# Performance work log

Measured on AMD Instinct MI355X. Metric: run time of the kernel, lower is better.

The kernel has to match this reference:

```python
import jax, jax.numpy as jnp
import numpy as np

N = 50000      # nodes
E = 800000     # edges (before self-loops)
IN = 128       # in_channels
HID = 32       # hidden_channels
H = 4          # num_heads
OUT = 2        # out_channels
NEG_SLOPE = 0.2


def setup_inputs() -> dict:
    key = jax.random.key(0)
    ks = jax.random.split(key, 16)
    s = 0.1
    x = jax.random.normal(ks[0], (N, IN), jnp.float32)
    edge_index = jax.random.randint(ks[1], (2, E), 0, N, dtype=jnp.int32)
    W1 = jax.random.normal(ks[2], (IN, H * HID), jnp.float32) * s
    att_src1 = jax.random.normal(ks[3], (H, HID), jnp.float32) * s
    att_dst1 = jax.random.normal(ks[4], (H, HID), jnp.float32) * s
    b1 = jnp.zeros((H * HID,), jnp.float32)
    W2 = jax.random.normal(ks[5], (H * HID, H * HID), jnp.float32) * s
    att_src2 = jax.random.normal(ks[6], (H, HID), jnp.float32) * s
    att_dst2 = jax.random.normal(ks[7], (H, HID), jnp.float32) * s
    b2 = jnp.zeros((H * HID,), jnp.float32)
    W3 = jax.random.normal(ks[8], (H * HID, OUT), jnp.float32) * s
    att_src3 = jax.random.normal(ks[9], (1, OUT), jnp.float32) * s
    att_dst3 = jax.random.normal(ks[10], (1, OUT), jnp.float32) * s
    b3 = jnp.zeros((OUT,), jnp.float32)
    return {"x": x, "edge_index": edge_index,
            "W1": W1, "att_src1": att_src1, "att_dst1": att_dst1, "b1": b1,
            "W2": W2, "att_src2": att_src2, "att_dst2": att_dst2, "b2": b2,
            "W3": W3, "att_src3": att_src3, "att_dst3": att_dst3, "b3": b3}


def gat_layer(x, src, dst, W, a_src, a_dst, b, heads, ch, concat):
    """PyG GATConv (eval mode): per-edge LeakyReLU attention, edge-softmax over
    incoming edges of each destination node, weighted scatter-add aggregation."""
    n = x.shape[0]
    h = (x @ W).reshape(n, heads, ch)                      # [N,H,C]
    alpha_s = jnp.sum(h * a_src, axis=-1)                  # [N,H]
    alpha_d = jnp.sum(h * a_dst, axis=-1)                  # [N,H]
    alpha = jax.nn.leaky_relu(alpha_s[src] + alpha_d[dst], NEG_SLOPE)  # [E',H]
    amax = jax.ops.segment_max(alpha, dst, num_segments=n)             # [N,H]
    e = jnp.exp(alpha - amax[dst])
    denom = jax.ops.segment_sum(e, dst, num_segments=n)
    w = e / denom[dst]                                     # softmax weights [E',H]
    out = jax.ops.segment_sum(h[src] * w[:, :, None], dst, num_segments=n)  # [N,H,C]
    out = out.reshape(n, heads * ch) if concat else out.mean(axis=1)
    return out + b


def reference(x, edge_index, W1, att_src1, att_dst1, b1,
              W2, att_src2, att_dst2, b2, W3, att_src3, att_dst3, b3):
    # PyG GATConv adds self-loops by default
    loop = jnp.arange(N, dtype=edge_index.dtype)
    src = jnp.concatenate([edge_index[0], loop])
    dst = jnp.concatenate([edge_index[1], loop])
    h = jax.nn.elu(gat_layer(x, src, dst, W1, att_src1, att_dst1, b1, H, HID, True))
    h = jax.nn.elu(gat_layer(h, src, dst, W2, att_src2, att_dst2, b2, H, HID, True))
    h = gat_layer(h, src, dst, W3, att_src3, att_dst3, b3, 1, OUT, False)
    return jax.nn.log_softmax(h, axis=1)
```

## Files before the change

kernel.cpp:

```cpp
#include <hip/hip_runtime.h>
#include <hip/hip_fp16.h>

#define NN 50000
#define EE 800000
#define ET 850000
#define NEG 0.2f
#define SCAN_B 1024
#define NBLK ((NN + SCAN_B - 1) / SCAN_B)
#define GHALF 391
#define RHALF 25024
#define HIST_BLKS ((ET + 255) / 256)

__device__ __forceinline__ float leaky(float x) { return fmaxf(x, NEG * x); }
__device__ __forceinline__ float elu_f(float x) { return x > 0.f ? x : expm1f(x); }

struct alignas(8) half4 { __half2 a, b; };

typedef _Float16 half8_t __attribute__((ext_vector_type(8)));
typedef float float4_t __attribute__((ext_vector_type(4)));

__device__ __forceinline__
void gemm_tile(const float* __restrict__ Xf, const __half* __restrict__ Xh,
               const __half* __restrict__ Wt, __half* __restrict__ Yh,
               int nrows, int row0, int lane,
               const float* __restrict__ att_s, const float* __restrict__ att_d,
               float* __restrict__ asb, float* __restrict__ adb) {
    int n = lane & 15, quad = lane >> 4;
    float atts_r[8], attd_r[8];
#pragma unroll
    for (int t = 0; t < 8; ++t) {
        atts_r[t] = att_s[t * 16 + n];
        attd_r[t] = att_d[t * 16 + n];
    }
    float4_t acc[8];
#pragma unroll
    for (int t = 0; t < 8; ++t) acc[t] = (float4_t){0.f, 0.f, 0.f, 0.f};
    int rA = row0 + n; if (rA >= nrows) rA = nrows - 1;
#pragma unroll
    for (int ch = 0; ch < 4; ++ch) {
        half8_t a;
        if (Xh) {
            a = *(const half8_t*)(Xh + (size_t)rA * 128 + ch * 32 + quad * 8);
        } else {
            const float* xp = Xf + (size_t)rA * 128 + ch * 32 + quad * 8;
            float4 f0 = *(const float4*)xp;
            float4 f1 = *(const float4*)(xp + 4);
            a = (half8_t){(_Float16)f0.x, (_Float16)f0.y, (_Float16)f0.z, (_Float16)f0.w,
                          (_Float16)f1.x, (_Float16)f1.y, (_Float16)f1.z, (_Float16)f1.w};
        }
#pragma unroll
        for (int t = 0; t < 8; ++t) {
            half8_t b = *(const half8_t*)(Wt + (t * 16 + n) * 128 + ch * 32 + quad * 8);
            acc[t] = __builtin_amdgcn_mfma_f32_16x16x32_f16(a, b, acc[t], 0, 0, 0);
        }
    }
#pragma unroll
    for (int rg = 0; rg < 4; ++rg) {
        int row = row0 + quad * 4 + rg;
        if (row < nrows) {
            __half* yp = Yh + (size_t)row * 128 + n;
#pragma unroll
            for (int t = 0; t < 8; ++t)
                yp[t * 16] = __float2half(acc[t][rg]);
        }
    }
#pragma unroll
    for (int rg = 0; rg < 4; ++rg) {
        float ps[4], pd[4];
#pragma unroll
        for (int h = 0; h < 4; ++h) {
            ps[h] = acc[2*h][rg] * atts_r[2*h] + acc[2*h+1][rg] * atts_r[2*h+1];
            pd[h] = acc[2*h][rg] * attd_r[2*h] + acc[2*h+1][rg] * attd_r[2*h+1];
#pragma unroll
            for (int mask = 1; mask < 16; mask <<= 1) {
                ps[h] += __shfl_xor(ps[h], mask, 64);
                pd[h] += __shfl_xor(pd[h], mask, 64);
            }
        }
        int row = row0 + quad * 4 + rg;
        if (n == 0 && row < nrows) {
#pragma unroll
            for (int h = 0; h < 4; ++h) {
                asb[row * 4 + h] = ps[h];
                adb[row * 4 + h] = pd[h];
            }
        }
    }
}

__global__ __launch_bounds__(256)
void gemm_mfma_k(const float* __restrict__ Xf, const __half* __restrict__ Xh,
                 const __half* __restrict__ Wt, __half* __restrict__ Yh, int nrows,
                 const float* __restrict__ att_s, const float* __restrict__ att_d,
                 float* __restrict__ asb, float* __restrict__ adb) {
    int lane = threadIdx.x & 63;
    int wid  = threadIdx.x >> 6;
    int row0 = (blockIdx.x * 4 + wid) * 16;
    if (row0 < nrows)
        gemm_tile(Xf, Xh, Wt, Yh, nrows, row0, lane, att_s, att_d, asb, adb);
}

__global__ __launch_bounds__(256)
void mega_k(const float* __restrict__ Xf, const __half* __restrict__ Wt,
            __half* __restrict__ Yh, int rowBase,
            const float* __restrict__ att_s, const float* __restrict__ att_d,
            float* __restrict__ asb, float* __restrict__ adb,
            int mode,
            const int* __restrict__ ei, int* __restrict__ counts,
            int* __restrict__ rank, const int* __restrict__ rp,
            int* __restrict__ csr) {
    int b = blockIdx.x;
    if (b < GHALF) {
        int lane = threadIdx.x & 63;
        int wid  = threadIdx.x >> 6;
        int row0 = rowBase + (b * 4 + wid) * 16;
        if (row0 < NN)
            gemm_tile(Xf, nullptr, Wt, Yh, NN, row0, lane, att_s, att_d, asb, adb);
    } else {
        int i = (b - GHALF) * 256 + threadIdx.x;
        if (i < ET) {
            if (mode == 0) {
                int dst = (i < EE) ? ei[EE + i] : (i - EE);
                rank[i] = atomicAdd(&counts[dst], 1);
            } else {
                int src, dst;
                if (i < EE) { src = ei[i]; dst = ei[EE + i]; }
                else        { src = dst = i - EE; }
                csr[rp[dst] + rank[i]] = src;
            }
        }
    }
}

__global__ void prep_k(const float* __restrict__ W1, __half* __restrict__ Wt1,
                       const float* __restrict__ W2, __half* __restrict__ Wt2,
                       int* __restrict__ counts) {
    int i = blockIdx.x * 256 + threadIdx.x;
    if (i < 16384) {
        int k = i >> 7, n = i & 127;
        Wt1[n * 128 + k] = __float2half(W1[i]);
    } else if (i < 32768) {
        int j = i - 16384;
        int k = j >> 7, n = j & 127;
        Wt2[n * 128 + k] = __float2half(W2[j]);
    } else {
        int j = i - 32768;
        if (j < NN) counts[j] = 0;
    }
}

__global__ void scan1_k(const int* __restrict__ counts, int* __restrict__ rp,
                        int* __restrict__ bsums) {
    __shared__ int lsum[256];
    int base = blockIdx.x * SCAN_B;
    int v[4];
    int tsum = 0;
#pragma unroll
    for (int j = 0; j < 4; ++j) {
        int i = base + threadIdx.x * 4 + j;
        v[j] = (i < NN) ? counts[i] : 0;
        tsum += v[j];
    }
    lsum[threadIdx.x] = tsum;
    __syncthreads();
    for (int off = 1; off < 256; off <<= 1) {
        int t = (threadIdx.x >= off) ? lsum[threadIdx.x - off] : 0;
        __syncthreads();
        lsum[threadIdx.x] += t;
        __syncthreads();
    }
    int excl = lsum[threadIdx.x] - tsum;
#pragma unroll
    for (int j = 0; j < 4; ++j) {
        int i = base + threadIdx.x * 4 + j;
        if (i < NN) rp[i] = excl;
        excl += v[j];
    }
    if (threadIdx.x == 255) bsums[blockIdx.x] = lsum[255];
}

__global__ void scan23_k(int* __restrict__ rp, const int* __restrict__ bsums) {
    __shared__ int sadd;
    int bx = blockIdx.x;
    if (threadIdx.x < 64) {
        int lane = threadIdx.x;
        int v = (lane < NBLK) ? bsums[lane] : 0;
        for (int off = 1; off < 64; off <<= 1) {
            int t = __shfl_up(v, off, 64);
            if (lane >= off) v += t;
        }
        int srcl = (bx == 0) ? 0 : (bx - 1);
        int ex = __shfl(v, srcl, 64);
        if (lane == 0) sadd = (bx == 0) ? 0 : ex;
        if (bx == 0 && lane == 63) rp[NN] = v;
    }
    __syncthreads();
    int add = sadd;
    int base = bx * SCAN_B + threadIdx.x * 4;
#pragma unroll
    for (int j = 0; j < 4; ++j) {
        int i = base + j;
        if (i < NN) rp[i] += add;
    }
}

__global__ __launch_bounds__(256)
void agg_k(const __half* __restrict__ Hh, const float* __restrict__ asb,
           const float* __restrict__ adb, const int* __restrict__ rp,
           const int* __restrict__ csr, const float* __restrict__ bias,
           __half* __restrict__ Y,
           const float* __restrict__ W3, const float* __restrict__ s3w,
           const float* __restrict__ d3w, float* __restrict__ h3,
           float* __restrict__ as3, float* __restrict__ ad3) {
    int lane = threadIdx.x & 63;
    int hw = lane >> 5;
    int l  = lane & 31;
    int n = blockIdx.x * 8 + (threadIdx.x >> 6) * 2 + hw;
    if (n >= NN) return;
    int hd = l >> 3;
    float ad = adb[n * 4 + hd];
    float acc0 = 0.f, acc1 = 0.f, acc2 = 0.f, acc3 = 0.f, den = 0.f;
    int e = rp[n], end = rp[n + 1], last = end - 1;
    for (int base = e; base < end; base += 8) {
        int s[8]; float a[8]; float2 hraw[8];
#pragma unroll
        for (int j = 0; j < 8; ++j) {
            int i = base + j;
            s[j] = csr[i <= last ? i : last];
        }
#pragma unroll
        for (int j = 0; j < 8; ++j) a[j] = asb[s[j] * 4 + hd] + ad;
#pragma unroll
        for (int j = 0; j < 8; ++j)
            hraw[j] = ((const float2*)(Hh + (size_t)s[j] * 128))[l];
#pragma unroll
        for (int j = 0; j < 8; ++j) {
            float w = __expf(leaky(a[j]));
            w = (base + j <= last) ? w : 0.f;
            den += w;
            const __half2* hp = (const __half2*)&hraw[j];
            float2 f01 = __half22float2(hp[0]);
            float2 f23 = __half22float2(hp[1]);
            acc0 += w * f01.x; acc1 += w * f01.y;
            acc2 += w * f23.x; acc3 += w * f23.y;
        }
    }
    float4 bv = ((const float4*)bias)[l];
    float inv = 1.f / den;
    float o0 = elu_f(acc0 * inv + bv.x);
    float o1 = elu_f(acc1 * inv + bv.y);
    float o2 = elu_f(acc2 * inv + bv.z);
    float o3 = elu_f(acc3 * inv + bv.w);
    if (!W3) {
        half4 hv;
        hv.a = __floats2half2_rn(o0, o1);
        hv.b = __floats2half2_rn(o2, o3);
        ((half4*)(Y + (size_t)n * 128))[l] = hv;
    } else {
        float4 wa = ((const float4*)W3)[l * 2];
        float4 wb = ((const float4*)W3)[l * 2 + 1];
        float p0 = o0 * wa.x + o1 * wa.z + o2 * wb.x + o3 * wb.z;
        float p1 = o0 * wa.y + o1 * wa.w + o2 * wb.y + o3 * wb.w;
        for (int off = 16; off > 0; off >>= 1) {
            p0 += __shfl_down(p0, off, 32);
            p1 += __shfl_down(p1, off, 32);
        }
        if (l == 0) {
            h3[n * 2 + 0] = p0;
            h3[n * 2 + 1] = p1;
            as3[n] = p0 * s3w[0] + p1 * s3w[1];
            ad3[n] = p0 * d3w[0] + p1 * d3w[1];
        }
    }
}

__global__ void l3agg_k(const float* __restrict__ h3, const float* __restrict__ as3,
                        const float* __restrict__ ad3, const int* __restrict__ rp,
                        const int* __restrict__ csr, const float* __restrict__ b3,
                        float* __restrict__ out) {
    int n = blockIdx.x * blockDim.x + threadIdx.x;
    if (n >= NN) return;
    const float2* h2 = (const float2*)h3;
    float adn = ad3[n];
    float den = 0.f, a0 = 0.f, a1 = 0.f;
    int e = rp[n], end = rp[n + 1], last = end - 1;
    for (int base = e; base < end; base += 4) {
        int s[4]; float al[4]; float2 g[4];
#pragma unroll
        for (int j = 0; j < 4; ++j) {
            int i = base + j;
            s[j] = csr[i <= last ? i : last];
        }
#pragma unroll
        for (int j = 0; j < 4; ++j) al[j] = as3[s[j]] + adn;
#pragma unroll
        for (int j = 0; j < 4; ++j) g[j] = h2[s[j]];
#pragma unroll
        for (int j = 0; j < 4; ++j) {
            float w = __expf(leaky(al[j]));
            w = (base + j <= last) ? w : 0.f;
            den += w;
            a0 += w * g[j].x;
            a1 += w * g[j].y;
        }
    }
    float o0 = a0 / den + b3[0];
    float o1 = a1 / den + b3[1];
    float m = fmaxf(o0, o1);
    float lse = m + logf(__expf(o0 - m) + __expf(o1 - m));
    out[n * 2 + 0] = o0 - lse;
    out[n * 2 + 1] = o1 - lse;
}

extern "C" void kernel_launch(void* const* d_in, const int* in_sizes, int n_in,
                              void* d_out, int out_size, void* d_ws, size_t ws_size,
                              hipStream_t stream) {
    const float* x   = (const float*)d_in[0];
    const int*   ei  = (const int*)d_in[1];
    const float* W1  = (const float*)d_in[2];
    const float* as1 = (const float*)d_in[3];
    const float* ad1 = (const float*)d_in[4];
    const float* b1  = (const float*)d_in[5];
    const float* W2  = (const float*)d_in[6];
    const float* as2 = (const float*)d_in[7];
    const float* ad2 = (const float*)d_in[8];
    const float* b2  = (const float*)d_in[9];
    const float* W3  = (const float*)d_in[10];
    const float* s3w = (const float*)d_in[11];
    const float* d3w = (const float*)d_in[12];
    const float* b3  = (const float*)d_in[13];
    float* out = (float*)d_out;

    char* ws = (char*)d_ws;
    size_t off = 0;
    auto alloc = [&](size_t bytes) -> char* {
        char* p = ws + off;
        off = (off + bytes + 255) & ~(size_t)255;
        return p;
    };
    __half* hA    = (__half*)alloc((size_t)NN * 128 * 2);
    __half* hBh   = (__half*)alloc((size_t)NN * 128 * 2);
    float* asb    = (float*)alloc((size_t)NN * 4 * 4);
    float* adb    = (float*)alloc((size_t)NN * 4 * 4);
    int*   rp     = (int*)alloc((size_t)(NN + 1) * 4);
    int*   counts = (int*)alloc((size_t)NN * 4);
    int*   csr    = (int*)alloc((size_t)ET * 4);
    int*   rank   = (int*)alloc((size_t)ET * 4);
    int*   bsums  = (int*)alloc((size_t)NBLK * 4);
    __half* Wt1   = (__half*)alloc(128 * 128 * 2);
    __half* Wt2   = (__half*)alloc(128 * 128 * 2);
    float* h3     = (float*)alloc((size_t)NN * 2 * 4);
    float* s3     = (float*)alloc((size_t)NN * 4);
    float* d3     = (float*)alloc((size_t)NN * 4);

    prep_k<<<(32768 + NN + 255) / 256, 256, 0, stream>>>(W1, Wt1, W2, Wt2, counts);

    mega_k<<<GHALF + HIST_BLKS, 256, 0, stream>>>(x, Wt1, hA, 0, as1, ad1, asb, adb,
                                                  0, ei, counts, rank, nullptr, nullptr);

    scan1_k<<<NBLK, 256, 0, stream>>>(counts, rp, bsums);
    scan23_k<<<NBLK, 256, 0, stream>>>(rp, bsums);

    mega_k<<<GHALF + HIST_BLKS, 256, 0, stream>>>(x, Wt1, hA, RHALF, as1, ad1, asb, adb,
                                                  1, ei, counts, rank, rp, csr);

    agg_k<<<(NN + 7) / 8, 256, 0, stream>>>(hA, asb, adb, rp, csr, b1, hBh,
                                            nullptr, nullptr, nullptr,
                                            nullptr, nullptr, nullptr);

    gemm_mfma_k<<<(NN + 63) / 64, 256, 0, stream>>>(nullptr, hBh, Wt2, hA, NN,
                                                    as2, ad2, asb, adb);

    agg_k<<<(NN + 7) / 8, 256, 0, stream>>>(hA, asb, adb, rp, csr, b2, nullptr,
                                            W3, s3w, d3w, h3, s3, d3);

    l3agg_k<<<(NN + 255) / 256, 256, 0, stream>>>(h3, s3, d3, rp, csr, b3, out);
}
```

Baseline: 268.3 us.

## Overlap layer-1 aggregation tail with layer-2 GEMM in a combined kernel

Layer-1 aggregation is split at node 39040: the first part runs alone, and the remaining nodes are aggregated in the same launch as GEMM tiles for rows already finished (rows below 39040). A final small GEMM launch covers the rest. New buffers hold layer-2 features and attention scores, since hA and asb/adb are still being read while the GEMM writes. The aim is to fill the idle tail of the aggregation and remove a dependency bubble, at the cost of extra workspace and hardcoded split constants.

```diff
diff --git a/kernel.cpp b/kernel.cpp
--- a/kernel.cpp
+++ b/kernel.cpp
@@ -10,6 +10,11 @@
 #define GHALF 391
 #define RHALF 25024
 #define HIST_BLKS ((ET + 255) / 256)
+#define NSPL 39040
+#define A1A_VB 4880
+#define A1B_VB 1370
+#define G2A 610
+#define G2B 172
 
 __device__ __forceinline__ float leaky(float x) { return fmaxf(x, NEG * x); }
 __device__ __forceinline__ float elu_f(float x) { return x > 0.f ? x : expm1f(x); }
@@ -88,14 +93,81 @@
     }
 }
 
+__device__ __forceinline__
+void agg_node(int n, int l, const __half* __restrict__ Hh,
+              const float* __restrict__ asb, const float* __restrict__ adb,
+              const int* __restrict__ rp, const int* __restrict__ csr,
+              const float* __restrict__ bias, __half* __restrict__ Y,
+              const float* __restrict__ W3, const float* __restrict__ s3w,
+              const float* __restrict__ d3w, float* __restrict__ h3,
+              float* __restrict__ as3, float* __restrict__ ad3) {
+    if (n >= NN) return;
+    int hd = l >> 3;
+    float ad = adb[n * 4 + hd];
+    float acc0 = 0.f, acc1 = 0.f, acc2 = 0.f, acc3 = 0.f, den = 0.f;
+    int e = rp[n], end = rp[n + 1], last = end - 1;
+    for (int base = e; base < end; base += 8) {
+        int s[8]; float a[8]; float2 hraw[8];
+#pragma unroll
+        for (int j = 0; j < 8; ++j) {
+            int i = base + j;
+            s[j] = csr[i <= last ? i : last];
+        }
+#pragma unroll
+        for (int j = 0; j < 8; ++j) a[j] = asb[s[j] * 4 + hd] + ad;
+#pragma unroll
+        for (int j = 0; j < 8; ++j)
+            hraw[j] = ((const float2*)(Hh + (size_t)s[j] * 128))[l];
+#pragma unroll
+        for (int j = 0; j < 8; ++j) {
+            float w = __expf(leaky(a[j]));
+            w = (base + j <= last) ? w : 0.f;
+            den += w;
+            const __half2* hp = (const __half2*)&hraw[j];
+            float2 f01 = __half22float2(hp[0]);
+            float2 f23 = __half22float2(hp[1]);
+            acc0 += w * f01.x; acc1 += w * f01.y;
+            acc2 += w * f23.x; acc3 += w * f23.y;
+        }
+    }
+    float4 bv = ((const float4*)bias)[l];
+    float inv = 1.f / den;
+    float o0 = elu_f(acc0 * inv + bv.x);
+    float o1 = elu_f(acc1 * inv + bv.y);
+    float o2 = elu_f(acc2 * inv + bv.z);
+    float o3 = elu_f(acc3 * inv + bv.w);
+    if (!W3) {
+        half4 hv;
+        hv.a = __floats2half2_rn(o0, o1);
+        hv.b = __floats2half2_rn(o2, o3);
+        ((half4*)(Y + (size_t)n * 128))[l] = hv;
+    } else {
+        float4 wa = ((const float4*)W3)[l * 2];
+        float4 wb = ((const float4*)W3)[l * 2 + 1];
+        float p0 = o0 * wa.x + o1 * wa.z + o2 * wb.x + o3 * wb.z;
+        float p1 = o0 * wa.y + o1 * wa.w + o2 * wb.y + o3 * wb.w;
+        for (int off = 16; off > 0; off >>= 1) {
+            p0 += __shfl_down(p0, off, 32);
+            p1 += __shfl_down(p1, off, 32);
+        }
+        if (l == 0) {
+            h3[n * 2 + 0] = p0;
+            h3[n * 2 + 1] = p1;
+            as3[n] = p0 * s3w[0] + p1 * s3w[1];
+            ad3[n] = p0 * d3w[0] + p1 * d3w[1];
+        }
+    }
+}
+
 __global__ __launch_bounds__(256)
 void gemm_mfma_k(const float* __restrict__ Xf, const __half* __restrict__ Xh,
                  const __half* __restrict__ Wt, __half* __restrict__ Yh, int nrows,
+                 int blk0,
                  const float* __restrict__ att_s, const float* __restrict__ att_d,
                  float* __restrict__ asb, float* __restrict__ adb) {
     int lane = threadIdx.x & 63;
     int wid  = threadIdx.x >> 6;
-    int row0 = (blockIdx.x * 4 + wid) * 16;
+    int row0 = ((blk0 + blockIdx.x) * 4 + wid) * 16;
     if (row0 < nrows)
         gemm_tile(Xf, Xh, Wt, Yh, nrows, row0, lane, att_s, att_d, asb, adb);
 }
@@ -132,6 +204,30 @@
     }
 }
 
+__global__ __launch_bounds__(256)
+void mega2_k(const __half* __restrict__ hA, const float* __restrict__ asb,
+             const float* __restrict__ adb, const int* __restrict__ rp,
+             const int* __restrict__ csr, const float* __restrict__ b1,
+             __half* __restrict__ hBh,
+             const __half* __restrict__ Wt2, __half* __restrict__ hC,
+             const float* __restrict__ as2, const float* __restrict__ ad2,
+             float* __restrict__ asb2, float* __restrict__ adb2) {
+    int b = blockIdx.x;
+    int lane = threadIdx.x & 63;
+    if (b < A1B_VB) {
+        int hw = lane >> 5;
+        int l  = lane & 31;
+        int n = NSPL + b * 8 + (threadIdx.x >> 6) * 2 + hw;
+        agg_node(n, l, hA, asb, adb, rp, csr, b1, hBh,
+                 nullptr, nullptr, nullptr, nullptr, nullptr, nullptr);
+    } else {
+        int g = b - A1B_VB;
+        int wid = threadIdx.x >> 6;
+        int row0 = (g * 4 + wid) * 16;
+        gemm_tile(nullptr, hBh, Wt2, hC, NN, row0, lane, as2, ad2, asb2, adb2);
+    }
+}
+
 __global__ void prep_k(const float* __restrict__ W1, __half* __restrict__ Wt1,
                        const float* __restrict__ W2, __half* __restrict__ Wt2,
                        int* __restrict__ counts) {
@@ -205,7 +301,7 @@
 }
 
 __global__ __launch_bounds__(256)
-void agg_k(const __half* __restrict__ Hh, const float* __restrict__ asb,
+void agg_k(int nb0, const __half* __restrict__ Hh, const float* __restrict__ asb,
            const float* __restrict__ adb, const int* __restrict__ rp,
            const int* __restrict__ csr, const float* __restrict__ bias,
            __half* __restrict__ Y,
@@ -215,63 +311,9 @@
     int lane = threadIdx.x & 63;
     int hw = lane >> 5;
     int l  = lane & 31;
-    int n = blockIdx.x * 8 + (threadIdx.x >> 6) * 2 + hw;
-    if (n >= NN) return;
-    int hd = l >> 3;
-    float ad = adb[n * 4 + hd];
-    float acc0 = 0.f, acc1 = 0.f, acc2 = 0.f, acc3 = 0.f, den = 0.f;
-    int e = rp[n], end = rp[n + 1], last = end - 1;
-    for (int base = e; base < end; base += 8) {
-        int s[8]; float a[8]; float2 hraw[8];
-#pragma unroll
-        for (int j = 0; j < 8; ++j) {
-            int i = base + j;
-            s[j] = csr[i <= last ? i : last];
-        }
-#pragma unroll
-        for (int j = 0; j < 8; ++j) a[j] = asb[s[j] * 4 + hd] + ad;
-#pragma unroll
-        for (int j = 0; j < 8; ++j)
-            hraw[j] = ((const float2*)(Hh + (size_t)s[j] * 128))[l];
-#pragma unroll
-        for (int j = 0; j < 8; ++j) {
-            float w = __expf(leaky(a[j]));
-            w = (base + j <= last) ? w : 0.f;
-            den += w;
-            const __half2* hp = (const __half2*)&hraw[j];
-            float2 f01 = __half22float2(hp[0]);
-            float2 f23 = __half22float2(hp[1]);
-            acc0 += w * f01.x; acc1 += w * f01.y;
-            acc2 += w * f23.x; acc3 += w * f23.y;
-        }
-    }
-    float4 bv = ((const float4*)bias)[l];
-    float inv = 1.f / den;
-    float o0 = elu_f(acc0 * inv + bv.x);
-    float o1 = elu_f(acc1 * inv + bv.y);
-    float o2 = elu_f(acc2 * inv + bv.z);
-    float o3 = elu_f(acc3 * inv + bv.w);
-    if (!W3) {
-        half4 hv;
-        hv.a = __floats2half2_rn(o0, o1);
-        hv.b = __floats2half2_rn(o2, o3);
-        ((half4*)(Y + (size_t)n * 128))[l] = hv;
-    } else {
-        float4 wa = ((const float4*)W3)[l * 2];
-        float4 wb = ((const float4*)W3)[l * 2 + 1];
-        float p0 = o0 * wa.x + o1 * wa.z + o2 * wb.x + o3 * wb.z;
-        float p1 = o0 * wa.y + o1 * wa.w + o2 * wb.y + o3 * wb.w;
-        for (int off = 16; off > 0; off >>= 1) {
-            p0 += __shfl_down(p0, off, 32);
-            p1 += __shfl_down(p1, off, 32);
-        }
-        if (l == 0) {
-            h3[n * 2 + 0] = p0;
-            h3[n * 2 + 1] = p1;
-            as3[n] = p0 * s3w[0] + p1 * s3w[1];
-            ad3[n] = p0 * d3w[0] + p1 * d3w[1];
-        }
-    }
+    int n = nb0 + blockIdx.x * 8 + (threadIdx.x >> 6) * 2 + hw;
+    agg_node(n, l, Hh, asb, adb, rp, csr, bias, Y,
+             W3, s3w, d3w, h3, as3, ad3);
 }
 
 __global__ void l3agg_k(const float* __restrict__ h3, const float* __restrict__ as3,
@@ -340,8 +382,11 @@
     };
     __half* hA    = (__half*)alloc((size_t)NN * 128 * 2);
     __half* hBh   = (__half*)alloc((size_t)NN * 128 * 2);
+    __half* hC    = (__half*)alloc((size_t)NN * 128 * 2);
     float* asb    = (float*)alloc((size_t)NN * 4 * 4);
     float* adb    = (float*)alloc((size_t)NN * 4 * 4);
+    float* asb2   = (float*)alloc((size_t)NN * 4 * 4);
+    float* adb2   = (float*)alloc((size_t)NN * 4 * 4);
     int*   rp     = (int*)alloc((size_t)(NN + 1) * 4);
     int*   counts = (int*)alloc((size_t)NN * 4);
     int*   csr    = (int*)alloc((size_t)ET * 4);
@@ -350,8 +395,8 @@
     __half* Wt1   = (__half*)alloc(128 * 128 * 2);
     __half* Wt2   = (__half*)alloc(128 * 128 * 2);
     float* h3     = (float*)alloc((size_t)NN * 2 * 4);
-    float* s3     = (float*)alloc((size_t)NN * 4);
-    float* d3     = (float*)alloc((size_t)NN * 4);
+    float* s3    = (float*)alloc((size_t)NN * 4);
+    float* d3    = (float*)alloc((size_t)NN * 4);
 
     prep_k<<<(32768 + NN + 255) / 256, 256, 0, stream>>>(W1, Wt1, W2, Wt2, counts);
 
@@ -364,14 +409,17 @@
     mega_k<<<GHALF + HIST_BLKS, 256, 0, stream>>>(x, Wt1, hA, RHALF, as1, ad1, asb, adb,
                                                   1, ei, counts, rank, rp, csr);
 
-    agg_k<<<(NN + 7) / 8, 256, 0, stream>>>(hA, asb, adb, rp, csr, b1, hBh,
-                                            nullptr, nullptr, nullptr,
-                                            nullptr, nullptr, nullptr);
-
-    gemm_mfma_k<<<(NN + 63) / 64, 256, 0, stream>>>(nullptr, hBh, Wt2, hA, NN,
-                                                    as2, ad2, asb, adb);
-
-    agg_k<<<(NN + 7) / 8, 256, 0, stream>>>(hA, asb, adb, rp, csr, b2, nullptr,
+    agg_k<<<A1A_VB, 256, 0, stream>>>(0, hA, asb, adb, rp, csr, b1, hBh,
+                                      nullptr, nullptr, nullptr,
+                                      nullptr, nullptr, nullptr);
+
+    mega2_k<<<A1B_VB + G2A, 256, 0, stream>>>(hA, asb, adb, rp, csr, b1, hBh,
+                                              Wt2, hC, as2, ad2, asb2, adb2);
+
+    gemm_mfma_k<<<G2B, 256, 0, stream>>>(nullptr, hBh, Wt2, hC, NN, G2A,
+                                         as2, ad2, asb2, adb2);
+
+    agg_k<<<(NN + 7) / 8, 256, 0, stream>>>(0, hC, asb2, adb2, rp, csr, b2, nullptr,
                                             W3, s3w, d3w, h3, s3, d3);
 
     l3agg_k<<<(NN + 255) / 256, 256, 0, stream>>>(h3, s3, d3, rp, csr, b3, out);
```

Result: no change. 271.5 us (+1.2%).

## Spread layer-1 GEMM across scan kernels and prefetch CSR indices in aggregation

Applied to the files above, without the earlier changes.

The layer-1 GEMM tiles are now spread over four launches (histogram, both scan phases, CSR fill). This fills the otherwise nearly idle scan kernels with useful GEMM work instead of splitting it evenly across two launches. The aggregation and layer-3 kernels software-pipeline the CSR neighbour index loads one batch of 8 ahead, and layer 3 widens its batch from 4 to 8. Layer 2 writes to separate buffers (hC, asb2, adb2), which removes buffer reuse hazards at the cost of extra workspace.

```diff
diff --git a/kernel.cpp b/kernel.cpp
--- a/kernel.cpp
+++ b/kernel.cpp
@@ -7,9 +7,10 @@
 #define NEG 0.2f
 #define SCAN_B 1024
 #define NBLK ((NN + SCAN_B - 1) / SCAN_B)
-#define GHALF 391
-#define RHALF 25024
 #define HIST_BLKS ((ET + 255) / 256)
+#define TA 300
+#define TS 100
+#define TB 282
 
 __device__ __forceinline__ float leaky(float x) { return fmaxf(x, NEG * x); }
 __device__ __forceinline__ float elu_f(float x) { return x > 0.f ? x : expm1f(x); }
@@ -88,47 +89,132 @@
     }
 }
 
-__global__ __launch_bounds__(256)
-void gemm_mfma_k(const float* __restrict__ Xf, const __half* __restrict__ Xh,
-                 const __half* __restrict__ Wt, __half* __restrict__ Yh, int nrows,
-                 const float* __restrict__ att_s, const float* __restrict__ att_d,
-                 float* __restrict__ asb, float* __restrict__ adb) {
-    int lane = threadIdx.x & 63;
-    int wid  = threadIdx.x >> 6;
-    int row0 = (blockIdx.x * 4 + wid) * 16;
-    if (row0 < nrows)
-        gemm_tile(Xf, Xh, Wt, Yh, nrows, row0, lane, att_s, att_d, asb, adb);
-}
-
-__global__ __launch_bounds__(256)
-void mega_k(const float* __restrict__ Xf, const __half* __restrict__ Wt,
-            __half* __restrict__ Yh, int rowBase,
-            const float* __restrict__ att_s, const float* __restrict__ att_d,
-            float* __restrict__ asb, float* __restrict__ adb,
-            int mode,
-            const int* __restrict__ ei, int* __restrict__ counts,
-            int* __restrict__ rank, const int* __restrict__ rp,
-            int* __restrict__ csr) {
-    int b = blockIdx.x;
-    if (b < GHALF) {
-        int lane = threadIdx.x & 63;
-        int wid  = threadIdx.x >> 6;
-        int row0 = rowBase + (b * 4 + wid) * 16;
-        if (row0 < NN)
-            gemm_tile(Xf, nullptr, Wt, Yh, NN, row0, lane, att_s, att_d, asb, adb);
-    } else {
-        int i = (b - GHALF) * 256 + threadIdx.x;
-        if (i < ET) {
-            if (mode == 0) {
-                int dst = (i < EE) ? ei[EE + i] : (i - EE);
-                rank[i] = atomicAdd(&counts[dst], 1);
-            } else {
-                int src, dst;
-                if (i < EE) { src = ei[i]; dst = ei[EE + i]; }
-                else        { src = dst = i - EE; }
-                csr[rp[dst] + rank[i]] = src;
-            }
-        }
+__device__ __forceinline__
+void agg_node(int n, int l, const __half* __restrict__ Hh,
+              const float* __restrict__ asb, const float* __restrict__ adb,
+              const int* __restrict__ rp, const int* __restrict__ csr,
+              const float* __restrict__ bias, __half* __restrict__ Y,
+              const float* __restrict__ W3, const float* __restrict__ s3w,
+              const float* __restrict__ d3w, float* __restrict__ h3,
+              float* __restrict__ as3, float* __restrict__ ad3) {
+    if (n >= NN) return;
+    int hd = l >> 3;
+    float ad = adb[n * 4 + hd];
+    float acc0 = 0.f, acc1 = 0.f, acc2 = 0.f, acc3 = 0.f, den = 0.f;
+    int e = rp[n], end = rp[n + 1], last = end - 1;
+    int s[8];
+#pragma unroll
+    for (int j = 0; j < 8; ++j) {
+        int i = e + j;
+        s[j] = csr[i <= last ? i : last];
+    }
+    for (int base = e; base < end; base += 8) {
+        float a[8]; float2 hraw[8]; int sN[8];
+#pragma unroll
+        for (int j = 0; j < 8; ++j)
+            hraw[j] = ((const float2*)(Hh + (size_t)s[j] * 128))[l];
+#pragma unroll
+        for (int j = 0; j < 8; ++j) a[j] = asb[s[j] * 4 + hd] + ad;
+        int nb = base + 8;
+#pragma unroll
+        for (int j = 0; j < 8; ++j) {
+            int i = nb + j;
+            sN[j] = csr[i <= last ? i : last];
+        }
+#pragma unroll
+        for (int j = 0; j < 8; ++j) {
+            float w = __expf(leaky(a[j]));
+            w = (base + j <= last) ? w : 0.f;
+            den += w;
+            const __half2* hp = (const __half2*)&hraw[j];
+            float2 f01 = __half22float2(hp[0]);
+            float2 f23 = __half22float2(hp[1]);
+            acc0 += w * f01.x; acc1 += w * f01.y;
+            acc2 += w * f23.x; acc3 += w * f23.y;
+        }
+#pragma unroll
+        for (int j = 0; j < 8; ++j) s[j] = sN[j];
+    }
+    float4 bv = ((const float4*)bias)[l];
+    float inv = 1.f / den;
+    float o0 = elu_f(acc0 * inv + bv.x);
+    float o1 = elu_f(acc1 * inv + bv.y);
+    float o2 = elu_f(acc2 * inv + bv.z);
+    float o3 = elu_f(acc3 * inv + bv.w);
+    if (!W3) {
+        half4 hv;
+        hv.a = __floats2half2_rn(o0, o1);
+        hv.b = __floats2half2_rn(o2, o3);
+        ((half4*)(Y + (size_t)n * 128))[l] = hv;
+    } else {
+        float4 wa = ((const float4*)W3)[l * 2];
+        float4 wb = ((const float4*)W3)[l * 2 + 1];
+        float p0 = o0 * wa.x + o1 * wa.z + o2 * wb.x + o3 * wb.z;
+        float p1 = o0 * wa.y + o1 * wa.w + o2 * wb.y + o3 * wb.w;
+        for (int off = 16; off > 0; off >>= 1) {
+            p0 += __shfl_down(p0, off, 32);
+            p1 += __shfl_down(p1, off, 32);
+        }
+        if (l == 0) {
+            h3[n * 2 + 0] = p0;
+            h3[n * 2 + 1] = p1;
+            as3[n] = p0 * s3w[0] + p1 * s3w[1];
+            ad3[n] = p0 * d3w[0] + p1 * d3w[1];
+        }
+    }
+}
+
+__device__ __forceinline__
+void scan1_f(const int* __restrict__ counts, int* __restrict__ rp,
+             int* __restrict__ bsums, int bx, int tid, int* lsum) {
+    int base = bx * SCAN_B;
+    int v[4]; int tsum = 0;
+#pragma unroll
+    for (int j = 0; j < 4; ++j) {
+        int i = base + tid * 4 + j;
+        v[j] = (i < NN) ? counts[i] : 0;
+        tsum += v[j];
+    }
+    lsum[tid] = tsum;
+    __syncthreads();
+    for (int off = 1; off < 256; off <<= 1) {
+        int t = (tid >= off) ? lsum[tid - off] : 0;
+        __syncthreads();
+        lsum[tid] += t;
+        __syncthreads();
+    }
+    int excl = lsum[tid] - tsum;
+#pragma unroll
+    for (int j = 0; j < 4; ++j) {
+        int i = base + tid * 4 + j;
+        if (i < NN) rp[i] = excl;
+        excl += v[j];
+    }
+    if (tid == 255) bsums[bx] = lsum[255];
+}
+
+__device__ __forceinline__
+void scan23_f(int* __restrict__ rp, const int* __restrict__ bsums,
+              int bx, int tid, int* psadd) {
+    if (tid < 64) {
+        int ln = tid;
+        int v = (ln < NBLK) ? bsums[ln] : 0;
+        for (int off = 1; off < 64; off <<= 1) {
+            int t = __shfl_up(v, off, 64);
+            if (ln >= off) v += t;
+        }
+        int srcl = (bx == 0) ? 0 : (bx - 1);
+        int ex = __shfl(v, srcl, 64);
+        if (ln == 0) *psadd = (bx == 0) ? 0 : ex;
+        if (bx == 0 && ln == 63) rp[NN] = v;
+    }
+    __syncthreads();
+    int add = *psadd;
+    int base = bx * SCAN_B + tid * 4;
+#pragma unroll
+    for (int j = 0; j < 4; ++j) {
+        int i = base + j;
+        if (i < NN) rp[i] += add;
     }
 }
 
@@ -149,59 +235,100 @@
     }
 }
 
-__global__ void scan1_k(const int* __restrict__ counts, int* __restrict__ rp,
-                        int* __restrict__ bsums) {
+__global__ __launch_bounds__(256)
+void megaA_k(const float* __restrict__ x, const __half* __restrict__ Wt1,
+             __half* __restrict__ hA,
+             const float* __restrict__ as1, const float* __restrict__ ad1,
+             float* __restrict__ asb, float* __restrict__ adb,
+             const int* __restrict__ ei, int* __restrict__ counts,
+             int* __restrict__ rank) {
+    int b = blockIdx.x;
+    if (b < TA) {
+        int lane = threadIdx.x & 63;
+        int wid  = threadIdx.x >> 6;
+        int row0 = (b * 4 + wid) * 16;
+        gemm_tile(x, nullptr, Wt1, hA, NN, row0, lane, as1, ad1, asb, adb);
+    } else {
+        int i = (b - TA) * 256 + threadIdx.x;
+        if (i < ET) {
+            int dst = (i < EE) ? ei[EE + i] : (i - EE);
+            rank[i] = atomicAdd(&counts[dst], 1);
+        }
+    }
+}
+
+__global__ __launch_bounds__(256)
+void megaS1_k(const int* __restrict__ counts, int* __restrict__ rp,
+              int* __restrict__ bsums,
+              const float* __restrict__ x, const __half* __restrict__ Wt1,
+              __half* __restrict__ hA,
+              const float* __restrict__ as1, const float* __restrict__ ad1,
+              float* __restrict__ asb, float* __restrict__ adb) {
     __shared__ int lsum[256];
-    int base = blockIdx.x * SCAN_B;
-    int v[4];
-    int tsum = 0;
-#pragma unroll
-    for (int j = 0; j < 4; ++j) {
-        int i = base + threadIdx.x * 4 + j;
-        v[j] = (i < NN) ? counts[i] : 0;
-        tsum += v[j];
-    }
-    lsum[threadIdx.x] = tsum;
-    __syncthreads();
-    for (int off = 1; off < 256; off <<= 1) {
-        int t = (threadIdx.x >= off) ? lsum[threadIdx.x - off] : 0;
-        __syncthreads();
-        lsum[threadIdx.x] += t;
-        __syncthreads();
-    }
-    int excl = lsum[threadIdx.x] - tsum;
-#pragma unroll
-    for (int j = 0; j < 4; ++j) {
-        int i = base + threadIdx.x * 4 + j;
-        if (i < NN) rp[i] = excl;
-        excl += v[j];
-    }
-    if (threadIdx.x == 255) bsums[blockIdx.x] = lsum[255];
-}
-
-__global__ void scan23_k(int* __restrict__ rp, const int* __restrict__ bsums) {
+    int b = blockIdx.x;
+    if (b < NBLK) {
+        scan1_f(counts, rp, bsums, b, threadIdx.x, lsum);
+    } else {
+        int lane = threadIdx.x & 63;
+        int wid  = threadIdx.x >> 6;
+        int row0 = ((TA + b - NBLK) * 4 + wid) * 16;
+        gemm_tile(x, nullptr, Wt1, hA, NN, row0, lane, as1, ad1, asb, adb);
+    }
+}
+
+__global__ __launch_bounds__(256)
+void megaS2_k(int* __restrict__ rp, const int* __restrict__ bsums,
+              const float* __restrict__ x, const __half* __restrict__ Wt1,
+              __half* __restrict__ hA,
+              const float* __restrict__ as1, const float* __restrict__ ad1,
+              float* __restrict__ asb, float* __restrict__ adb) {
     __shared__ int sadd;
-    int bx = blockIdx.x;
-    if (threadIdx.x < 64) {
-        int lane = threadIdx.x;
-        int v = (lane < NBLK) ? bsums[lane] : 0;
-        for (int off = 1; off < 64; off <<= 1) {
-            int t = __shfl_up(v, off, 64);
-            if (lane >= off) v += t;
-        }
-        int srcl = (bx == 0) ? 0 : (bx - 1);
-        int ex = __shfl(v, srcl, 64);
-        if (lane == 0) sadd = (bx == 0) ? 0 : ex;
-        if (bx == 0 && lane == 63) rp[NN] = v;
-    }
-    __syncthreads();
-    int add = sadd;
-    int base = bx * SCAN_B + threadIdx.x * 4;
-#pragma unroll
-    for (int j = 0; j < 4; ++j) {
-        int i = base + j;
-        if (i < NN) rp[i] += add;
-    }
+    int b = blockIdx.x;
+    if (b < NBLK) {
+        scan23_f(rp, bsums, b, threadIdx.x, &sadd);
+    } else {
+        int lane = threadIdx.x & 63;
+        int wid  = threadIdx.x >> 6;
+        int row0 = ((TA + TS + b - NBLK) * 4 + wid) * 16;
+        gemm_tile(x, nullptr, Wt1, hA, NN, row0, lane, as1, ad1, asb, adb);
+    }
+}
+
+__global__ __launch_bounds__(256)
+void megaB_k(const float* __restrict__ x, const __half* __restrict__ Wt1,
+             __half* __restrict__ hA,
+             const float* __restrict__ as1, const float* __restrict__ ad1,
+             float* __restrict__ asb, float* __restrict__ adb,
+             const int* __restrict__ ei, const int* __restrict__ rp,
+             const int* __restrict__ rank, int* __restrict__ csr) {
+    int b = blockIdx.x;
+    if (b < TB) {
+        int lane = threadIdx.x & 63;
+        int wid  = threadIdx.x >> 6;
+        int row0 = ((TA + 2 * TS + b) * 4 + wid) * 16;
+        if (row0 < NN)
+            gemm_tile(x, nullptr, Wt1, hA, NN, row0, lane, as1, ad1, asb, adb);
+    } else {
+        int i = (b - TB) * 256 + threadIdx.x;
+        if (i < ET) {
+            int src, dst;
+            if (i < EE) { src = ei[i]; dst = ei[EE + i]; }
+            else        { src = dst = i - EE; }
+            csr[rp[dst] + rank[i]] = src;
+        }
+    }
+}
+
+__global__ __launch_bounds__(256)
+void gemm_mfma_k(const __half* __restrict__ Xh, const __half* __restrict__ Wt,
+                 __half* __restrict__ Yh,
+                 const float* __restrict__ att_s, const float* __restrict__ att_d,
+                 float* __restrict__ asb, float* __restrict__ adb) {
+    int lane = threadIdx.x & 63;
+    int wid  = threadIdx.x >> 6;
+    int row0 = (blockIdx.x * 4 + wid) * 16;
+    if (row0 < NN)
+        gemm_tile(nullptr, Xh, Wt, Yh, NN, row0, lane, att_s, att_d, asb, adb);
 }
 
 __global__ __launch_bounds__(256)
@@ -216,62 +343,8 @@
     int hw = lane >> 5;
     int l  = lane & 31;
     int n = blockIdx.x * 8 + (threadIdx.x >> 6) * 2 + hw;
-    if (n >= NN) return;
-    int hd = l >> 3;
-    float ad = adb[n * 4 + hd];
-    float acc0 = 0.f, acc1 = 0.f, acc2 = 0.f, acc3 = 0.f, den = 0.f;
-    int e = rp[n], end = rp[n + 1], last = end - 1;
-    for (int base = e; base < end; base += 8) {
-        int s[8]; float a[8]; float2 hraw[8];
-#pragma unroll
-        for (int j = 0; j < 8; ++j) {
-            int i = base + j;
-            s[j] = csr[i <= last ? i : last];
-        }
-#pragma unroll
-        for (int j = 0; j < 8; ++j) a[j] = asb[s[j] * 4 + hd] + ad;
-#pragma unroll
-        for (int j = 0; j < 8; ++j)
-            hraw[j] = ((const float2*)(Hh + (size_t)s[j] * 128))[l];
-#pragma unroll
-        for (int j = 0; j < 8; ++j) {
-            float w = __expf(leaky(a[j]));
-            w = (base + j <= last) ? w : 0.f;
-            den += w;
-            const __half2* hp = (const __half2*)&hraw[j];
-            float2 f01 = __half22float2(hp[0]);
-            float2 f23 = __half22float2(hp[1]);
-            acc0 += w * f01.x; acc1 += w * f01.y;
-            acc2 += w * f23.x; acc3 += w * f23.y;
-        }
-    }
-    float4 bv = ((const float4*)bias)[l];
-    float inv = 1.f / den;
-    float o0 = elu_f(acc0 * inv + bv.x);
-    float o1 = elu_f(acc1 * inv + bv.y);
-    float o2 = elu_f(acc2 * inv + bv.z);
-    float o3 = elu_f(acc3 * inv + bv.w);
-    if (!W3) {
-        half4 hv;
-        hv.a = __floats2half2_rn(o0, o1);
-        hv.b = __floats2half2_rn(o2, o3);
-        ((half4*)(Y + (size_t)n * 128))[l] = hv;
-    } else {
-        float4 wa = ((const float4*)W3)[l * 2];
-        float4 wb = ((const float4*)W3)[l * 2 + 1];
-        float p0 = o0 * wa.x + o1 * wa.z + o2 * wb.x + o3 * wb.z;
-        float p1 = o0 * wa.y + o1 * wa.w + o2 * wb.y + o3 * wb.w;
-        for (int off = 16; off > 0; off >>= 1) {
-            p0 += __shfl_down(p0, off, 32);
-            p1 += __shfl_down(p1, off, 32);
-        }
-        if (l == 0) {
-            h3[n * 2 + 0] = p0;
-            h3[n * 2 + 1] = p1;
-            as3[n] = p0 * s3w[0] + p1 * s3w[1];
-            ad3[n] = p0 * d3w[0] + p1 * d3w[1];
-        }
-    }
+    agg_node(n, l, Hh, asb, adb, rp, csr, bias, Y,
+             W3, s3w, d3w, h3, as3, ad3);
 }
 
 __global__ void l3agg_k(const float* __restrict__ h3, const float* __restrict__ as3,
@@ -284,25 +357,34 @@
     float adn = ad3[n];
     float den = 0.f, a0 = 0.f, a1 = 0.f;
     int e = rp[n], end = rp[n + 1], last = end - 1;
-    for (int base = e; base < end; base += 4) {
-        int s[4]; float al[4]; float2 g[4];
-#pragma unroll
-        for (int j = 0; j < 4; ++j) {
-            int i = base + j;
-            s[j] = csr[i <= last ? i : last];
-        }
-#pragma unroll
-        for (int j = 0; j < 4; ++j) al[j] = as3[s[j]] + adn;
-#pragma unroll
-        for (int j = 0; j < 4; ++j) g[j] = h2[s[j]];
-#pragma unroll
-        for (int j = 0; j < 4; ++j) {
+    int s[8];
+#pragma unroll
+    for (int j = 0; j < 8; ++j) {
+        int i = e + j;
+        s[j] = csr[i <= last ? i : last];
+    }
+    for (int base = e; base < end; base += 8) {
+        float al[8]; float2 g[8]; int sN[8];
+#pragma unroll
+        for (int j = 0; j < 8; ++j) g[j] = h2[s[j]];
+#pragma unroll
+        for (int j = 0; j < 8; ++j) al[j] = as3[s[j]] + adn;
+        int nb = base + 8;
+#pragma unroll
+        for (int j = 0; j < 8; ++j) {
+            int i = nb + j;
+            sN[j] = csr[i <= last ? i : last];
+        }
+#pragma unroll
+        for (int j = 0; j < 8; ++j) {
             float w = __expf(leaky(al[j]));
             w = (base + j <= last) ? w : 0.f;
             den += w;
             a0 += w * g[j].x;
             a1 += w * g[j].y;
         }
+#pragma unroll
+        for (int j = 0; j < 8; ++j) s[j] = sN[j];
     }
     float o0 = a0 / den + b3[0];
     float o1 = a1 / den + b3[1];
@@ -340,8 +422,11 @@
     };
     __half* hA    = (__half*)alloc((size_t)NN * 128 * 2);
     __half* hBh   = (__half*)alloc((size_t)NN * 128 * 2);
+    __half* hC    = (__half*)alloc((size_t)NN * 128 * 2);
     float* asb    = (float*)alloc((size_t)NN * 4 * 4);
     float* adb    = (float*)alloc((size_t)NN * 4 * 4);
+    float* asb2   = (float*)alloc((size_t)NN * 4 * 4);
+    float* adb2   = (float*)alloc((size_t)NN * 4 * 4);
     int*   rp     = (int*)alloc((size_t)(NN + 1) * 4);
     int*   counts = (int*)alloc((size_t)NN * 4);
     int*   csr    = (int*)alloc((size_t)ET * 4);
@@ -355,23 +440,26 @@
 
     prep_k<<<(32768 + NN + 255) / 256, 256, 0, stream>>>(W1, Wt1, W2, Wt2, counts);
 
-    mega_k<<<GHALF + HIST_BLKS, 256, 0, stream>>>(x, Wt1, hA, 0, as1, ad1, asb, adb,
-                                                  0, ei, counts, rank, nullptr, nullptr);
-
-    scan1_k<<<NBLK, 256, 0, stream>>>(counts, rp, bsums);
-    scan23_k<<<NBLK, 256, 0, stream>>>(rp, bsums);
-
-    mega_k<<<GHALF + HIST_BLKS, 256, 0, stream>>>(x, Wt1, hA, RHALF, as1, ad1, asb, adb,
-                                                  1, ei, counts, rank, rp, csr);
+    megaA_k<<<TA + HIST_BLKS, 256, 0, stream>>>(x, Wt1, hA, as1, ad1, asb, adb,
+                                                ei, counts, rank);
+
+    megaS1_k<<<NBLK + TS, 256, 0, stream>>>(counts, rp, bsums,
+                                            x, Wt1, hA, as1, ad1, asb, adb);
+
+    megaS2_k<<<NBLK + TS, 256, 0, stream>>>(rp, bsums,
+                                            x, Wt1, hA, as1, ad1, asb, adb);
+
+    megaB_k<<<TB + HIST_BLKS, 256, 0, stream>>>(x, Wt1, hA, as1, ad1, asb, adb,
+                                                ei, rp, rank, csr);
 
     agg_k<<<(NN + 7) / 8, 256, 0, stream>>>(hA, asb, adb, rp, csr, b1, hBh,
                                             nullptr, nullptr, nullptr,
                                             nullptr, nullptr, nullptr);
 
-    gemm_mfma_k<<<(NN + 63) / 64, 256, 0, stream>>>(nullptr, hBh, Wt2, hA, NN,
-                                                    as2, ad2, asb, adb);
-
-    agg_k<<<(NN + 7) / 8, 256, 0, stream>>>(hA, asb, adb, rp, csr, b2, nullptr,
+    gemm_mfma_k<<<(NN + 63) / 64, 256, 0, stream>>>(hBh, Wt2, hC,
+                                                    as2, ad2, asb2, adb2);
+
+    agg_k<<<(NN + 7) / 8, 256, 0, stream>>>(hC, asb2, adb2, rp, csr, b2, nullptr,
                                             W3, s3w, d3w, h3, s3, d3);
 
     l3agg_k<<<(NN + 255) / 256, 256, 0, stream>>>(h3, s3, d3, rp, csr, b3, out);
```

Result: slower. 275.9 us (+2.8%).
